# Kernel optimization log

Hardware: AMD Instinct MI355X
Metric: run time of the kernel (lower is better)

Reference implementation:

```python
import jax, jax.numpy as jnp
import numpy as np

D_MODEL = 1024
NUM_HEADS = 16
HEAD_DIM = D_MODEL // NUM_HEADS
SEQ_LEN = 4096
BATCH = 1
ROPE_THETA = 10000.0


def apply_rope(x, theta):
    # x: [B, H, S, D], interleaved pair rotation (x_{2i}, x_{2i+1})
    D = x.shape[-1]
    S = x.shape[-2]
    pos = jnp.arange(S, dtype=jnp.float32)
    inv_freq = theta ** (-jnp.arange(0, D, 2, dtype=jnp.float32) / D)  # [D/2]
    ang = pos[:, None] * inv_freq[None, :]  # [S, D/2]
    cos = jnp.cos(ang).astype(x.dtype)
    sin = jnp.sin(ang).astype(x.dtype)
    x1 = x[..., 0::2]
    x2 = x[..., 1::2]
    r1 = x1 * cos - x2 * sin
    r2 = x1 * sin + x2 * cos
    return jnp.stack([r1, r2], axis=-1).reshape(x.shape)


def setup_inputs() -> dict:
    key = jax.random.key(0)
    ks = jax.random.split(key, 5)
    s = 1.0 / np.sqrt(D_MODEL)
    return {
        "x": jax.random.normal(ks[0], (BATCH, SEQ_LEN, D_MODEL), jnp.float32),
        "Wq": jax.random.normal(ks[1], (D_MODEL, D_MODEL), jnp.float32) * s,
        "Wk": jax.random.normal(ks[2], (D_MODEL, D_MODEL), jnp.float32) * s,
        "Wv": jax.random.normal(ks[3], (D_MODEL, D_MODEL), jnp.float32) * s,
        "Wo": jax.random.normal(ks[4], (D_MODEL, D_MODEL), jnp.float32) * s,
    }


def reference(x, Wq, Wk, Wv, Wo):
    B, S, _ = x.shape
    # bias-free linear: y = x @ W.T
    def proj(W):
        y = jnp.einsum('bsd,ed->bse', x, W)
        return y.reshape(B, S, NUM_HEADS, HEAD_DIM).transpose(0, 2, 1, 3)  # [B,H,S,hd]
    q = apply_rope(proj(Wq), ROPE_THETA)
    k = apply_rope(proj(Wk), ROPE_THETA)
    v = proj(Wv)
    scale = 1.0 / jnp.sqrt(jnp.asarray(HEAD_DIM, dtype=x.dtype))
    scores = jnp.einsum('bhqd,bhkd->bhqk', q, k) * scale  # [B,H,S,S]
    causal = jnp.tril(jnp.ones((S, S), dtype=bool))
    scores = jnp.where(causal, scores, jnp.asarray(-jnp.inf, dtype=scores.dtype))
    attn = jax.nn.softmax(scores, axis=-1)
    out = jnp.einsum('bhqk,bhkd->bhqd', attn, v)
    out = out.transpose(0, 2, 1, 3).reshape(B, S, D_MODEL)
    return jnp.einsum('bsd,ed->bse', out, Wo)
```

## Files before the change

### kernel.cpp

```cpp
#include <hip/hip_runtime.h>
#include <math.h>

#define SEQ 4096
#define DM  1024
#define NH  16

typedef __attribute__((ext_vector_type(8))) short bf16x8;
typedef __attribute__((ext_vector_type(4))) float f32x4;
typedef __attribute__((ext_vector_type(16))) float f32x16;
typedef __attribute__((ext_vector_type(4))) unsigned int u32x4;

#define QSCALE 0.18033688011112042f

__device__ __forceinline__ unsigned short f2bf(float f){
  unsigned int u = __float_as_uint(f);
  u += 0x7fffu + ((u >> 16) & 1u);
  return (unsigned short)(u >> 16);
}

__device__ __forceinline__ unsigned int cvtpk(float lo, float hi){
  unsigned int r;
  asm("v_cvt_pk_bf16_f32 %0, %1, %2" : "=v"(r) : "v"(lo), "v"(hi));
  return r;
}

__device__ __forceinline__ void gload_lds16(const void* g, void* l){
  __builtin_amdgcn_global_load_lds(
      (const __attribute__((address_space(1))) unsigned int*)g,
      (__attribute__((address_space(3))) unsigned int*)l,
      16, 0, 0);
}

__global__ __launch_bounds__(256) void prep_kernel(const float* __restrict__ x,
                                                   const float* __restrict__ Wq, const float* __restrict__ Wk,
                                                   const float* __restrict__ Wv, const float* __restrict__ Wo,
                                                   unsigned short* __restrict__ xb,
                                                   unsigned short* __restrict__ wqb, unsigned short* __restrict__ wkb,
                                                   unsigned short* __restrict__ wvb, unsigned short* __restrict__ wob,
                                                   float2* __restrict__ ropetab){
  const int sel = blockIdx.y;
  if (sel < 5){
    const float* src = (sel == 0) ? x : (sel == 1) ? Wq : (sel == 2) ? Wk : (sel == 3) ? Wv : Wo;
    unsigned short* dst = (sel == 0) ? xb : (sel == 1) ? wqb : (sel == 2) ? wkb : (sel == 3) ? wvb : wob;
    const int n4 = (sel == 0) ? SEQ * DM / 4 : DM * DM / 4;
    int i = blockIdx.x * 256 + threadIdx.x;
    int stride = gridDim.x * 256;
    for (; i < n4; i += stride){
      float4 v = ((const float4*)src)[i];
      ushort4 o; o.x = f2bf(v.x); o.y = f2bf(v.y); o.z = f2bf(v.z); o.w = f2bf(v.w);
      ((ushort4*)dst)[i] = o;
    }
  } else {
    int i = blockIdx.x * 256 + threadIdx.x;
    int stride = gridDim.x * 256;
    for (; i < SEQ * 32; i += stride){
      int f = i >> 12, s = i & 4095;
      double inv = exp2(-(double)f * (13.287712379549449 / 32.0));
      double a = (double)s * inv;
      const double twopi = 6.283185307179586476;
      a -= twopi * floor(a / twopi);
      float af = (float)a;
      ropetab[i] = make_float2(cosf(af), sinf(af));
    }
  }
}

__global__ __launch_bounds__(256) void qkv_gemm(const unsigned short* __restrict__ A,
                                                const unsigned short* __restrict__ Wq,
                                                const unsigned short* __restrict__ Wk,
                                                const unsigned short* __restrict__ Wv,
                                                unsigned short* __restrict__ Qo,
                                                unsigned short* __restrict__ Ko,
                                                unsigned short* __restrict__ Vto,
                                                const float2* __restrict__ rope)
{
  __shared__ unsigned short At[128 * 64];
  __shared__ unsigned short Bt[128 * 64];
  const int sel = blockIdx.x >> 3;
  const unsigned short* B = (sel == 0) ? Wq : (sel == 1) ? Wk : Wv;
  const int K = DM;
  const int t = threadIdx.x;
  const int lane = t & 63, w = t >> 6;
  const int lg = lane >> 4, lr = lane & 15;
  const int wr = w >> 1, wc = w & 1;
  const int m0 = blockIdx.y * 128, n0 = (blockIdx.x & 7) * 128;

  f32x4 acc[4][4];
  #pragma unroll
  for (int mi = 0; mi < 4; mi++)
    #pragma unroll
    for (int nj = 0; nj < 4; nj++)
      acc[mi][nj] = (f32x4){0.f, 0.f, 0.f, 0.f};

  for (int k0 = 0; k0 < K; k0 += 64){
    __syncthreads();
    #pragma unroll
    for (int r = 0; r < 4; r++){
      int idx = r * 256 + t, row = idx >> 3, ch = idx & 7, cs = ch ^ (row & 7);
      gload_lds16(&A[(size_t)(m0 + row) * K + k0 + cs * 8], &At[idx * 8]);
    }
    #pragma unroll
    for (int r = 0; r < 4; r++){
      int idx = r * 256 + t, row = idx >> 3, ch = idx & 7, cs = ch ^ (row & 7);
      gload_lds16(&B[(size_t)(n0 + row) * K + k0 + cs * 8], &Bt[idx * 8]);
    }
    __syncthreads();
    #pragma unroll
    for (int kk = 0; kk < 2; kk++){
      bf16x8 af[4], bfr[4];
      #pragma unroll
      for (int mi = 0; mi < 4; mi++){
        int row = wr * 64 + mi * 16 + lr;
        af[mi] = *(const bf16x8*)&At[row * 64 + (((kk * 4 + lg) ^ (row & 7)) << 3)];
      }
      #pragma unroll
      for (int nj = 0; nj < 4; nj++){
        int row = wc * 64 + nj * 16 + lr;
        bfr[nj] = *(const bf16x8*)&Bt[row * 64 + (((kk * 4 + lg) ^ (row & 7)) << 3)];
      }
      #pragma unroll
      for (int mi = 0; mi < 4; mi++)
        #pragma unroll
        for (int nj = 0; nj < 4; nj++)
          acc[mi][nj] = __builtin_amdgcn_mfma_f32_16x16x32_bf16(af[mi], bfr[nj], acc[mi][nj], 0, 0, 0);
    }
  }

  #pragma unroll
  for (int mi = 0; mi < 4; mi++){
    #pragma unroll
    for (int nj = 0; nj < 4; nj++){
      f32x4 v = acc[mi][nj];
      int col  = n0 + wc * 64 + nj * 16 + lr;
      int row0 = m0 + wr * 64 + mi * 16 + lg * 4;
      if (sel == 0){
        int i = (col & 63) >> 1;
        const float4* tp = (const float4*)&rope[(size_t)i * SEQ + row0];
        float4 cA = tp[0], cB = tp[1];
        float cj[4] = {cA.x, cA.z, cB.x, cB.z};
        float sj[4] = {cA.y, cA.w, cB.y, cB.w};
        #pragma unroll
        for (int j = 0; j < 4; j++){
          float val = v[j];
          float oth = __shfl_xor(val, 1);
          int row = row0 + j;
          float res = ((col & 1) == 0) ? (val * cj[j] - oth * sj[j])
                                       : (oth * sj[j] + val * cj[j]);
          Qo[(size_t)row * DM + col] = f2bf(res * QSCALE);
        }
      } else if (sel == 1){
        const int hh = col >> 6, d = col & 63;
        int i = d >> 1;
        const float4* tp = (const float4*)&rope[(size_t)i * SEQ + row0];
        float4 cA = tp[0], cB = tp[1];
        float cj[4] = {cA.x, cA.z, cB.x, cB.z};
        float sj[4] = {cA.y, cA.w, cB.y, cB.w};
        #pragma unroll
        for (int j = 0; j < 4; j++){
          float val = v[j];
          float oth = __shfl_xor(val, 1);
          int row = row0 + j;
          float res = ((d & 1) == 0) ? (val * cj[j] - oth * sj[j])
                                     : (oth * sj[j] + val * cj[j]);
          size_t idx = ((size_t)((hh * 128 + (row >> 5)) * 8 + (d >> 3))) * 256
                       + (row & 31) * 8 + (d & 7);
          Ko[idx] = f2bf(res);
        }
      } else {
        const int hh = col >> 6, d = col & 63;
        ushort4 pkv; pkv.x = f2bf(v[0]); pkv.y = f2bf(v[1]); pkv.z = f2bf(v[2]); pkv.w = f2bf(v[3]);
        size_t idx = ((size_t)(((hh * 2 + (d >> 5)) * 64 + (row0 >> 6)) * 8 + ((row0 >> 3) & 7))) * 256
                     + (d & 31) * 8 + (row0 & 7);
        *(ushort4*)&Vto[idx] = pkv;
      }
    }
  }
}

__global__ __launch_bounds__(256) void gemm_out(const unsigned short* __restrict__ A,
                                                const unsigned short* __restrict__ B,
                                                float* __restrict__ C)
{
  __shared__ unsigned short At[128 * 64];
  __shared__ unsigned short Bt[64 * 64];
  const int K = DM;
  const int t = threadIdx.x;
  const int lane = t & 63, w = t >> 6;
  const int lg = lane >> 4, lr = lane & 15;
  const int wr = w >> 1, wc = w & 1;
  const int m0 = blockIdx.y * 128, n0 = blockIdx.x * 64;

  f32x4 acc[4][2];
  #pragma unroll
  for (int mi = 0; mi < 4; mi++)
    #pragma unroll
    for (int nj = 0; nj < 2; nj++)
      acc[mi][nj] = (f32x4){0.f, 0.f, 0.f, 0.f};

  for (int k0 = 0; k0 < K; k0 += 64){
    __syncthreads();
    #pragma unroll
    for (int r = 0; r < 4; r++){
      int idx = r * 256 + t, row = idx >> 3, ch = idx & 7, cs = ch ^ (row & 7);
      gload_lds16(&A[(size_t)(m0 + row) * K + k0 + cs * 8], &At[idx * 8]);
    }
    #pragma unroll
    for (int r = 0; r < 2; r++){
      int idx = r * 256 + t, row = idx >> 3, ch = idx & 7, cs = ch ^ (row & 7);
      gload_lds16(&B[(size_t)(n0 + row) * K + k0 + cs * 8], &Bt[idx * 8]);
    }
    __syncthreads();
    #pragma unroll
    for (int kk = 0; kk < 2; kk++){
      bf16x8 af[4], bfr[2];
      #pragma unroll
      for (int mi = 0; mi < 4; mi++){
        int row = wr * 64 + mi * 16 + lr;
        af[mi] = *(const bf16x8*)&At[row * 64 + (((kk * 4 + lg) ^ (row & 7)) << 3)];
      }
      #pragma unroll
      for (int nj = 0; nj < 2; nj++){
        int row = wc * 32 + nj * 16 + lr;
        bfr[nj] = *(const bf16x8*)&Bt[row * 64 + (((kk * 4 + lg) ^ (row & 7)) << 3)];
      }
      #pragma unroll
      for (int mi = 0; mi < 4; mi++)
        #pragma unroll
        for (int nj = 0; nj < 2; nj++)
          acc[mi][nj] = __builtin_amdgcn_mfma_f32_16x16x32_bf16(af[mi], bfr[nj], acc[mi][nj], 0, 0, 0);
    }
  }

  #pragma unroll
  for (int mi = 0; mi < 4; mi++)
    #pragma unroll
    for (int nj = 0; nj < 2; nj++){
      f32x4 v = acc[mi][nj];
      int col  = n0 + wc * 32 + nj * 16 + lr;
      int row0 = m0 + wr * 64 + mi * 16 + lg * 4;
      #pragma unroll
      for (int j = 0; j < 4; j++)
        C[(size_t)(row0 + j) * DM + col] = v[j];
    }
}

__global__ __launch_bounds__(256, 4) void attn5_kernel(const unsigned short* __restrict__ Qb,
                                                       const unsigned short* __restrict__ Kp,
                                                       const unsigned short* __restrict__ Vp,
                                                       unsigned short* __restrict__ AO)
{
  __shared__ unsigned int oS[3][16][2][32];
  __shared__ float lS[3][32];

  const int h = blockIdx.x;
  const int qi = (int)gridDim.y - 1 - (int)blockIdx.y;
  const int q0 = qi * 32;
  const int t = threadIdx.x, w = t >> 6, lane = t & 63;
  const int ql = lane & 31, hi = lane >> 5;
  const int qrow = q0 + ql;

  const int nkt = (qi >> 1) + 1;

  bf16x8 qf[4];
  #pragma unroll
  for (int ds = 0; ds < 4; ds++)
    qf[ds] = *(const bf16x8*)&Qb[(size_t)qrow * DM + h * 64 + ds * 16 + hi * 8];

  f32x16 oacc[2];
  #pragma unroll
  for (int d = 0; d < 2; d++)
    #pragma unroll
    for (int r = 0; r < 16; r++) oacc[d][r] = 0.f;
  float lrun = 0.f;

  f32x16 zv;
  #pragma unroll
  for (int r = 0; r < 16; r++) zv[r] = 0.f;

  const bf16x8* Kf = (const bf16x8*)Kp + (size_t)h * 128 * 8 * 32;
  const bf16x8* Vf = (const bf16x8*)Vp + (size_t)h * 2 * 64 * 8 * 32;

  for (int kt = w; kt < nkt; kt += 4){
    const int k0 = kt << 6;
    const bool diag = (kt == nkt - 1);

    __builtin_amdgcn_s_setprio(1);
    f32x16 s0, s1;
    {
      bf16x8 kf[4];
      #pragma unroll
      for (int ds = 0; ds < 4; ds++)
        kf[ds] = Kf[(size_t)((kt * 2 + 0) * 8 + ds * 2 + hi) * 32 + ql];
      s0 = __builtin_amdgcn_mfma_f32_32x32x16_bf16(kf[0], qf[0], zv, 0, 0, 0);
      #pragma unroll
      for (int ds = 1; ds < 4; ds++)
        s0 = __builtin_amdgcn_mfma_f32_32x32x16_bf16(kf[ds], qf[ds], s0, 0, 0, 0);
    }
    {
      bf16x8 kf[4];
      #pragma unroll
      for (int ds = 0; ds < 4; ds++)
        kf[ds] = Kf[(size_t)((kt * 2 + 1) * 8 + ds * 2 + hi) * 32 + ql];
      s1 = __builtin_amdgcn_mfma_f32_32x32x16_bf16(kf[0], qf[0], zv, 0, 0, 0);
      #pragma unroll
      for (int ds = 1; ds < 4; ds++)
        s1 = __builtin_amdgcn_mfma_f32_32x32x16_bf16(kf[ds], qf[ds], s1, 0, 0, 0);
    }
    __builtin_amdgcn_s_setprio(0);

    if (diag){
      #pragma unroll
      for (int r = 0; r < 16; r++){
        int keyb = k0 + (r & 3) + 8 * (r >> 2) + 4 * hi;
        if (keyb > qrow)      s0[r] = -INFINITY;
        if (keyb + 32 > qrow) s1[r] = -INFINITY;
      }
    }

    float ts0 = 0.f, ts1 = 0.f, ts2 = 0.f, ts3 = 0.f;
    #pragma unroll
    for (int i = 0; i < 16; i += 4){
      s0[i]     = __builtin_amdgcn_exp2f(s0[i]);     ts0 += s0[i];
      s0[i + 1] = __builtin_amdgcn_exp2f(s0[i + 1]); ts1 += s0[i + 1];
      s0[i + 2] = __builtin_amdgcn_exp2f(s0[i + 2]); ts2 += s0[i + 2];
      s0[i + 3] = __builtin_amdgcn_exp2f(s0[i + 3]); ts3 += s0[i + 3];
    }
    #pragma unroll
    for (int i = 0; i < 16; i += 4){
      s1[i]     = __builtin_amdgcn_exp2f(s1[i]);     ts0 += s1[i];
      s1[i + 1] = __builtin_amdgcn_exp2f(s1[i + 1]); ts1 += s1[i + 1];
      s1[i + 2] = __builtin_amdgcn_exp2f(s1[i + 2]); ts2 += s1[i + 2];
      s1[i + 3] = __builtin_amdgcn_exp2f(s1[i + 3]); ts3 += s1[i + 3];
    }
    float ts = (ts0 + ts1) + (ts2 + ts3);
    ts += __shfl_xor(ts, 32);
    lrun += ts;

    u32x4 pfr[4];
    #pragma unroll
    for (int ks = 0; ks < 4; ks++){
      const f32x16& sv = (ks < 2) ? s0 : s1;
      int b = (ks & 1) * 8;
      unsigned int a  = cvtpk(sv[b + 0], sv[b + 1]);
      unsigned int c  = cvtpk(sv[b + 2], sv[b + 3]);
      unsigned int bb = cvtpk(sv[b + 4], sv[b + 5]);
      unsigned int d  = cvtpk(sv[b + 6], sv[b + 7]);
      unsigned int sa = (unsigned int)__shfl_xor((int)a, 32);
      unsigned int sc = (unsigned int)__shfl_xor((int)c, 32);
      unsigned int sb = (unsigned int)__shfl_xor((int)bb, 32);
      unsigned int sd = (unsigned int)__shfl_xor((int)d, 32);
      pfr[ks][0] = hi ? sb : a;
      pfr[ks][1] = hi ? sd : c;
      pfr[ks][2] = hi ? bb : sa;
      pfr[ks][3] = hi ? d  : sc;
    }

    __builtin_amdgcn_s_setprio(1);
    #pragma unroll
    for (int dcol = 0; dcol < 2; dcol++){
      bf16x8 vf[4];
      #pragma unroll
      for (int ks = 0; ks < 4; ks++)
        vf[ks] = Vf[(size_t)((dcol * 64 + kt) * 8 + ks * 2 + hi) * 32 + ql];
      #pragma unroll
      for (int ks = 0; ks < 4; ks++){
        union { u32x4 u; bf16x8 v; } pf; pf.u = pfr[ks];
        oacc[dcol] = __builtin_amdgcn_mfma_f32_32x32x16_bf16(pf.v, vf[ks], oacc[dcol], 0, 0, 0);
      }
    }
    __builtin_amdgcn_s_setprio(0);
  }

  if (w > 0){
    if (hi == 0) lS[w - 1][ql] = lrun;
    #pragma unroll
    for (int r = 0; r < 16; r++)
      oS[w - 1][r][hi][ql] = cvtpk(oacc[0][r], oacc[1][r]);
  }
  __syncthreads();
  if (w == 0){
    float lstar = lrun + lS[0][ql] + lS[1][ql] + lS[2][ql];
    float rl = 1.f / lstar;
    #pragma unroll
    for (int r = 0; r < 16; r++){
      int rowloc = (r & 3) + 8 * (r >> 2) + 4 * hi;
      float rr = __shfl(rl, rowloc);
      int row = q0 + rowloc;
      float o0 = oacc[0][r], o1 = oacc[1][r];
      #pragma unroll
      for (int j = 0; j < 3; j++){
        unsigned int u = oS[j][r][hi][ql];
        o0 += __uint_as_float(u << 16);
        o1 += __uint_as_float(u & 0xffff0000u);
      }
      AO[(size_t)row * DM + h * 64 + ql]      = f2bf(o0 * rr);
      AO[(size_t)row * DM + h * 64 + 32 + ql] = f2bf(o1 * rr);
    }
  }
}

extern "C" void kernel_launch(void* const* d_in, const int* in_sizes, int n_in,
                              void* d_out, int out_size, void* d_ws, size_t ws_size,
                              hipStream_t stream)
{
  const float* x  = (const float*)d_in[0];
  const float* Wq = (const float*)d_in[1];
  const float* Wk = (const float*)d_in[2];
  const float* Wv = (const float*)d_in[3];
  const float* Wo = (const float*)d_in[4];

  char* ws = (char*)d_ws;
  unsigned short* xb  = (unsigned short*)ws; ws += (size_t)SEQ * DM * 2;
  unsigned short* wqb = (unsigned short*)ws; ws += (size_t)DM * DM * 2;
  unsigned short* wkb = (unsigned short*)ws; ws += (size_t)DM * DM * 2;
  unsigned short* wvb = (unsigned short*)ws; ws += (size_t)DM * DM * 2;
  unsigned short* wob = (unsigned short*)ws; ws += (size_t)DM * DM * 2;
  unsigned short* Qb  = (unsigned short*)ws; ws += (size_t)SEQ * DM * 2;
  unsigned short* Kpr = (unsigned short*)ws; ws += (size_t)SEQ * DM * 2;
  unsigned short* Vpr = (unsigned short*)ws; ws += (size_t)DM * SEQ * 2;
  unsigned short* AO  = (unsigned short*)ws; ws += (size_t)SEQ * DM * 2;
  float2* ropetab     = (float2*)ws;         ws += (size_t)SEQ * 32 * sizeof(float2);

  prep_kernel<<<dim3(512, 6), 256, 0, stream>>>(x, Wq, Wk, Wv, Wo,
                                                xb, wqb, wkb, wvb, wob, ropetab);

  qkv_gemm<<<dim3(24, 32), 256, 0, stream>>>(xb, wqb, wkb, wvb, Qb, Kpr, Vpr, ropetab);

  attn5_kernel<<<dim3(NH, SEQ / 32), 256, 0, stream>>>(Qb, Kpr, Vpr, AO);

  gemm_out<<<dim3(16, 32), 256, 0, stream>>>(AO, wob, (float*)d_out);
}
```

Measured before the change: 136.2 us.

## Double-buffer LDS tiles with K=32 steps in QKV and output GEMMs

Both projection GEMMs now keep two LDS buffers of 32-wide K tiles. The next tile's global-to-LDS load is issued before the MFMA work on the current tile, so one barrier per step replaces the previous two-barrier load-then-compute pattern. A new 4-chunk XOR swizzle fits the narrower tile rows. The aim is to hide global load latency behind matrix math. The cost is twice as many loop iterations with less work per barrier, plus an explicit vmcnt(0) wait each step.

```diff
diff --git a/kernel.cpp b/kernel.cpp
--- a/kernel.cpp
+++ b/kernel.cpp
@@ -65,6 +65,8 @@
   }
 }
 
+__device__ __forceinline__ int swz32(int row){ return (row ^ (row >> 2)) & 3; }
+
 __global__ __launch_bounds__(256) void qkv_gemm(const unsigned short* __restrict__ A,
                                                 const unsigned short* __restrict__ Wq,
                                                 const unsigned short* __restrict__ Wk,
@@ -74,8 +76,8 @@
                                                 unsigned short* __restrict__ Vto,
                                                 const float2* __restrict__ rope)
 {
-  __shared__ unsigned short At[128 * 64];
-  __shared__ unsigned short Bt[128 * 64];
+  __shared__ unsigned short At[2][128 * 32];
+  __shared__ unsigned short Bt[2][128 * 32];
   const int sel = blockIdx.x >> 3;
   const unsigned short* B = (sel == 0) ? Wq : (sel == 1) ? Wk : Wv;
   const int K = DM;
@@ -92,38 +94,46 @@
     for (int nj = 0; nj < 4; nj++)
       acc[mi][nj] = (f32x4){0.f, 0.f, 0.f, 0.f};
 
-  for (int k0 = 0; k0 < K; k0 += 64){
-    __syncthreads();
-    #pragma unroll
-    for (int r = 0; r < 4; r++){
-      int idx = r * 256 + t, row = idx >> 3, ch = idx & 7, cs = ch ^ (row & 7);
-      gload_lds16(&A[(size_t)(m0 + row) * K + k0 + cs * 8], &At[idx * 8]);
-    }
-    #pragma unroll
-    for (int r = 0; r < 4; r++){
-      int idx = r * 256 + t, row = idx >> 3, ch = idx & 7, cs = ch ^ (row & 7);
-      gload_lds16(&B[(size_t)(n0 + row) * K + k0 + cs * 8], &Bt[idx * 8]);
-    }
-    __syncthreads();
-    #pragma unroll
-    for (int kk = 0; kk < 2; kk++){
-      bf16x8 af[4], bfr[4];
-      #pragma unroll
-      for (int mi = 0; mi < 4; mi++){
-        int row = wr * 64 + mi * 16 + lr;
-        af[mi] = *(const bf16x8*)&At[row * 64 + (((kk * 4 + lg) ^ (row & 7)) << 3)];
-      }
-      #pragma unroll
-      for (int nj = 0; nj < 4; nj++){
-        int row = wc * 64 + nj * 16 + lr;
-        bfr[nj] = *(const bf16x8*)&Bt[row * 64 + (((kk * 4 + lg) ^ (row & 7)) << 3)];
-      }
-      #pragma unroll
-      for (int mi = 0; mi < 4; mi++)
-        #pragma unroll
-        for (int nj = 0; nj < 4; nj++)
-          acc[mi][nj] = __builtin_amdgcn_mfma_f32_16x16x32_bf16(af[mi], bfr[nj], acc[mi][nj], 0, 0, 0);
-    }
+  auto stage = [&](int buf, int k0){
+    #pragma unroll
+    for (int r = 0; r < 2; r++){
+      int idx = r * 256 + t, row = idx >> 2, ch = idx & 3, cs = ch ^ swz32(row);
+      gload_lds16(&A[(size_t)(m0 + row) * K + k0 + cs * 8], &At[buf][idx * 8]);
+    }
+    #pragma unroll
+    for (int r = 0; r < 2; r++){
+      int idx = r * 256 + t, row = idx >> 2, ch = idx & 3, cs = ch ^ swz32(row);
+      gload_lds16(&B[(size_t)(n0 + row) * K + k0 + cs * 8], &Bt[buf][idx * 8]);
+    }
+  };
+
+  stage(0, 0);
+  asm volatile("s_waitcnt vmcnt(0)" ::: "memory");
+  __builtin_amdgcn_s_barrier();
+
+  for (int step = 0; step < 32; step++){
+    const int buf = step & 1;
+    if (step + 1 < 32) stage(buf ^ 1, (step + 1) * 32);
+
+    bf16x8 af[4], bfr[4];
+    #pragma unroll
+    for (int mi = 0; mi < 4; mi++){
+      int row = wr * 64 + mi * 16 + lr;
+      af[mi] = *(const bf16x8*)&At[buf][row * 32 + ((lg ^ swz32(row)) << 3)];
+    }
+    #pragma unroll
+    for (int nj = 0; nj < 4; nj++){
+      int row = wc * 64 + nj * 16 + lr;
+      bfr[nj] = *(const bf16x8*)&Bt[buf][row * 32 + ((lg ^ swz32(row)) << 3)];
+    }
+    #pragma unroll
+    for (int mi = 0; mi < 4; mi++)
+      #pragma unroll
+      for (int nj = 0; nj < 4; nj++)
+        acc[mi][nj] = __builtin_amdgcn_mfma_f32_16x16x32_bf16(af[mi], bfr[nj], acc[mi][nj], 0, 0, 0);
+
+    asm volatile("s_waitcnt vmcnt(0)" ::: "memory");
+    __builtin_amdgcn_s_barrier();
   }
 
   #pragma unroll
@@ -181,8 +191,8 @@
                                                 const unsigned short* __restrict__ B,
                                                 float* __restrict__ C)
 {
-  __shared__ unsigned short At[128 * 64];
-  __shared__ unsigned short Bt[64 * 64];
+  __shared__ unsigned short At[2][128 * 32];
+  __shared__ unsigned short Bt[2][64 * 32];
   const int K = DM;
   const int t = threadIdx.x;
   const int lane = t & 63, w = t >> 6;
@@ -197,38 +207,45 @@
     for (int nj = 0; nj < 2; nj++)
       acc[mi][nj] = (f32x4){0.f, 0.f, 0.f, 0.f};
 
-  for (int k0 = 0; k0 < K; k0 += 64){
-    __syncthreads();
-    #pragma unroll
-    for (int r = 0; r < 4; r++){
-      int idx = r * 256 + t, row = idx >> 3, ch = idx & 7, cs = ch ^ (row & 7);
-      gload_lds16(&A[(size_t)(m0 + row) * K + k0 + cs * 8], &At[idx * 8]);
-    }
+  auto stage = [&](int buf, int k0){
     #pragma unroll
     for (int r = 0; r < 2; r++){
-      int idx = r * 256 + t, row = idx >> 3, ch = idx & 7, cs = ch ^ (row & 7);
-      gload_lds16(&B[(size_t)(n0 + row) * K + k0 + cs * 8], &Bt[idx * 8]);
-    }
-    __syncthreads();
-    #pragma unroll
-    for (int kk = 0; kk < 2; kk++){
-      bf16x8 af[4], bfr[2];
-      #pragma unroll
-      for (int mi = 0; mi < 4; mi++){
-        int row = wr * 64 + mi * 16 + lr;
-        af[mi] = *(const bf16x8*)&At[row * 64 + (((kk * 4 + lg) ^ (row & 7)) << 3)];
-      }
-      #pragma unroll
-      for (int nj = 0; nj < 2; nj++){
-        int row = wc * 32 + nj * 16 + lr;
-        bfr[nj] = *(const bf16x8*)&Bt[row * 64 + (((kk * 4 + lg) ^ (row & 7)) << 3)];
-      }
-      #pragma unroll
-      for (int mi = 0; mi < 4; mi++)
-        #pragma unroll
-        for (int nj = 0; nj < 2; nj++)
-          acc[mi][nj] = __builtin_amdgcn_mfma_f32_16x16x32_bf16(af[mi], bfr[nj], acc[mi][nj], 0, 0, 0);
-    }
+      int idx = r * 256 + t, row = idx >> 2, ch = idx & 3, cs = ch ^ swz32(row);
+      gload_lds16(&A[(size_t)(m0 + row) * K + k0 + cs * 8], &At[buf][idx * 8]);
+    }
+    {
+      int idx = t, row = idx >> 2, ch = idx & 3, cs = ch ^ swz32(row);
+      gload_lds16(&B[(size_t)(n0 + row) * K + k0 + cs * 8], &Bt[buf][idx * 8]);
+    }
+  };
+
+  stage(0, 0);
+  asm volatile("s_waitcnt vmcnt(0)" ::: "memory");
+  __builtin_amdgcn_s_barrier();
+
+  for (int step = 0; step < 32; step++){
+    const int buf = step & 1;
+    if (step + 1 < 32) stage(buf ^ 1, (step + 1) * 32);
+
+    bf16x8 af[4], bfr[2];
+    #pragma unroll
+    for (int mi = 0; mi < 4; mi++){
+      int row = wr * 64 + mi * 16 + lr;
+      af[mi] = *(const bf16x8*)&At[buf][row * 32 + ((lg ^ swz32(row)) << 3)];
+    }
+    #pragma unroll
+    for (int nj = 0; nj < 2; nj++){
+      int row = wc * 32 + nj * 16 + lr;
+      bfr[nj] = *(const bf16x8*)&Bt[buf][row * 32 + ((lg ^ swz32(row)) << 3)];
+    }
+    #pragma unroll
+    for (int mi = 0; mi < 4; mi++)
+      #pragma unroll
+      for (int nj = 0; nj < 2; nj++)
+        acc[mi][nj] = __builtin_amdgcn_mfma_f32_16x16x32_bf16(af[mi], bfr[nj], acc[mi][nj], 0, 0, 0);
+
+    asm volatile("s_waitcnt vmcnt(0)" ::: "memory");
+    __builtin_amdgcn_s_barrier();
   }
 
   #pragma unroll
```

Measured after the change: 135.6 us. Within noise of the previous version (-0.5%).
